# Optimization experiments

Measured on AMD Instinct MI355X. Metric: run time of the kernel, lower is better.

Reference implementation:

```python
import jax, jax.numpy as jnp
import numpy as np

E_DIM = 640   # RNA-FM embedding dim
H = 256       # hidden_dim
L = 3         # num_gcn_layers
LN_EPS = 1e-5


def _layer_norm(x, g, b):
    mu = jnp.mean(x, axis=-1, keepdims=True)
    var = jnp.mean((x - mu) ** 2, axis=-1, keepdims=True)
    return (x - mu) * jax.lax.rsqrt(var + LN_EPS) * g + b


def setup_inputs() -> dict:
    key = jax.random.key(0)
    ks = jax.random.split(key, 20)
    B, S = 4, 256

    def w(k, shape):
        fan_in = shape[-2] if len(shape) >= 2 else shape[-1]
        return jax.random.normal(k, shape, dtype=jnp.float32) / np.sqrt(fan_in)

    inp = {
        "embeddings": jax.random.normal(ks[0], (B, S, E_DIM), dtype=jnp.float32),
        "bp_priors": jax.random.uniform(ks[1], (B, S, S), dtype=jnp.float32),
        "sequence_lengths": jnp.full((B,), S, dtype=jnp.int32),
        # FeatureEncoder: Linear(640, 512) -> ReLU -> Linear(512, 256)
        "enc_w1": w(ks[2], (E_DIM, 2 * H)), "enc_b1": jnp.zeros((2 * H,), jnp.float32),
        "enc_w2": w(ks[3], (2 * H, H)),     "enc_b2": jnp.zeros((H,), jnp.float32),
        # GCN layers (stacked over L)
        "gcn_wself": w(ks[4], (L, H, H)), "gcn_bself": jnp.zeros((L, H), jnp.float32),
        "gcn_wedge": w(ks[5], (L, H, H)), "gcn_bedge": jnp.zeros((L, H), jnp.float32),
        "gcn_ln_g": jnp.ones((L, H), jnp.float32), "gcn_ln_b": jnp.zeros((L, H), jnp.float32),
        # PairwiseScorer MLP: Linear(2H+1, H) -> ReLU -> Linear(H, H//2) -> ReLU -> Linear(H//2, 1)
        "mlp_w1": w(ks[6], (2 * H + 1, H)), "mlp_b1": jnp.zeros((H,), jnp.float32),
        "mlp_w2": w(ks[7], (H, H // 2)),    "mlp_b2": jnp.zeros((H // 2,), jnp.float32),
        "mlp_w3": w(ks[8], (H // 2, 1)),    "mlp_b3": jnp.zeros((1,), jnp.float32),
    }
    return inp


def reference(embeddings, bp_priors, sequence_lengths,
              enc_w1, enc_b1, enc_w2, enc_b2,
              gcn_wself, gcn_bself, gcn_wedge, gcn_bedge, gcn_ln_g, gcn_ln_b,
              mlp_w1, mlp_b1, mlp_w2, mlp_b2, mlp_w3, mlp_b3):
    # FeatureEncoder
    h = jax.nn.relu(embeddings @ enc_w1 + enc_b1) @ enc_w2 + enc_b2  # [B,S,H]

    # GCN layers: self GEMM + adjacency (bp_priors) aggregated neighbor GEMM
    for l in range(L):
        self_f = h @ gcn_wself[l] + gcn_bself[l]
        neigh_f = jnp.einsum('bij,bjh->bih', bp_priors, h @ gcn_wedge[l] + gcn_bedge[l])
        h = _layer_norm(jax.nn.relu(self_f + neigh_f), gcn_ln_g[l], gcn_ln_b[l])

    # PairwiseScorer: concat([node_i, node_j, prior]) @ W1 split into three partial products
    # (mathematically identical to the expand-concat-MLP in the torch module).
    hi = h @ mlp_w1[:H]           # [B,S,H] contribution of node_i
    hj = h @ mlp_w1[H:2 * H]      # [B,S,H] contribution of node_j
    p = jax.nn.relu(hi[:, :, None, :] + hj[:, None, :, :]
                    + bp_priors[..., None] * mlp_w1[2 * H] + mlp_b1)  # [B,S,S,H]
    p = jax.nn.relu(p @ mlp_w2 + mlp_b2)                              # [B,S,S,H//2]
    bp_scores = (p @ mlp_w3 + mlp_b3)[..., 0]                         # [B,S,S]
    return bp_scores
```

## Files before the change

### kernel.cpp

```cpp
#include <hip/hip_runtime.h>

typedef __attribute__((ext_vector_type(8))) short short8;
typedef __attribute__((ext_vector_type(4))) float f32x4;

__device__ __forceinline__ unsigned short f2bf(float x) {
    union { float f; unsigned u; } v; v.f = x;
    unsigned r = v.u + 0x7FFF + ((v.u >> 16) & 1);
    return (unsigned short)(r >> 16);
}
__device__ __forceinline__ float bf2f(unsigned short h) {
    union { unsigned u; float f; } v; v.u = ((unsigned)h) << 16;
    return v.f;
}

template<bool RELU>
__global__ __launch_bounds__(256)
void gemm32(const float* __restrict__ A, const float* __restrict__ B0,
            const float* __restrict__ bias0, float* __restrict__ C0,
            const float* __restrict__ B1, const float* __restrict__ bias1,
            float* __restrict__ C1,
            int M, int N, int K, int aB, int bB, int cB, int nxHalf)
{
    int bx = blockIdx.x;
    const float* B = B0; const float* bias = bias0; float* C = C0;
    if (nxHalf && bx >= nxHalf) { bx -= nxHalf; B = B1; bias = bias1; C = C1; }
    A += (long)blockIdx.z * aB;
    B += (long)blockIdx.z * bB;
    C += (long)blockIdx.z * cB;
    const int m0 = blockIdx.y * 32, n0 = bx * 64;

    __shared__ __align__(16) float As[32][36];
    __shared__ __align__(16) float Bs[32][68];
    const int tid = threadIdx.x;
    const int tx = tid & 15, ty = tid >> 4;
    float acc[2][4] = {};

    for (int k0 = 0; k0 < K; k0 += 32) {
        {
            int row = tid >> 3, kq = (tid & 7) << 2;
            float4 v = *(const float4*)&A[(long)(m0 + row) * K + k0 + kq];
            As[kq + 0][row] = v.x; As[kq + 1][row] = v.y;
            As[kq + 2][row] = v.z; As[kq + 3][row] = v.w;
        }
#pragma unroll
        for (int q = 0; q < 2; ++q) {
            int f = tid * 2 + q;
            int kk = f >> 4, nn = (f & 15) << 2;
            *(float4*)&Bs[kk][nn] = *(const float4*)&B[(long)(k0 + kk) * N + n0 + nn];
        }
        __syncthreads();
#pragma unroll
        for (int k = 0; k < 32; ++k) {
            float2 a2 = *(const float2*)&As[k][ty * 2];
            float4 b4 = *(const float4*)&Bs[k][tx * 4];
            acc[0][0] += a2.x * b4.x; acc[0][1] += a2.x * b4.y;
            acc[0][2] += a2.x * b4.z; acc[0][3] += a2.x * b4.w;
            acc[1][0] += a2.y * b4.x; acc[1][1] += a2.y * b4.y;
            acc[1][2] += a2.y * b4.z; acc[1][3] += a2.y * b4.w;
        }
        __syncthreads();
    }

#pragma unroll
    for (int i = 0; i < 2; ++i) {
        int m = m0 + ty * 2 + i;
#pragma unroll
        for (int j = 0; j < 4; ++j) {
            int n = n0 + tx * 4 + j;
            float v = acc[i][j];
            if (bias) v += bias[n];
            if (RELU) v = fmaxf(v, 0.f);
            C[(long)m * N + n] = v;
        }
    }
}

__global__ __launch_bounds__(256)
void add_relu_ln(const float* __restrict__ a, const float* __restrict__ b,
                 const float* __restrict__ g, const float* __restrict__ bb,
                 float* __restrict__ o)
{
    const int row = blockIdx.x, t = threadIdx.x;
    const long idx = (long)row * 256 + t;
    float x = fmaxf(a[idx] + b[idx], 0.f);
    float s = x, s2 = x * x;
#pragma unroll
    for (int off = 1; off < 64; off <<= 1) {
        s  += __shfl_xor(s,  off, 64);
        s2 += __shfl_xor(s2, off, 64);
    }
    __shared__ float ws1[4], ws2[4];
    const int wid = t >> 6, lane = t & 63;
    if (lane == 0) { ws1[wid] = s; ws2[wid] = s2; }
    __syncthreads();
    s  = ws1[0] + ws1[1] + ws1[2] + ws1[3];
    s2 = ws2[0] + ws2[1] + ws2[2] + ws2[3];
    const float mu  = s * (1.f / 256.f);
    const float var = s2 * (1.f / 256.f) - mu * mu;
    o[idx] = (x - mu) * rsqrtf(var + 1e-5f) * g[t] + bb[t];
}

__global__ __launch_bounds__(256)
void split_w2t(const float* __restrict__ w2, short* __restrict__ w2th,
               short* __restrict__ w2tl)
{
    int e = blockIdx.x * 256 + threadIdx.x;
    int k = e >> 7, n = e & 127;
    float x = w2[k * 128 + n];
    unsigned short h = f2bf(x);
    unsigned short lo = f2bf(x - bf2f(h));
    w2th[n * 256 + k] = (short)h;
    w2tl[n * 256 + k] = (short)lo;
}

__global__ __launch_bounds__(256)
void pairwise_mfma(const float* __restrict__ hia, const float* __restrict__ hja,
                   const float* __restrict__ bp,
                   const float* __restrict__ c,
                   const float* __restrict__ b1,
                   const short* __restrict__ w2th, const short* __restrict__ w2tl,
                   const float* __restrict__ b2,
                   const float* __restrict__ w3,
                   const float* __restrict__ b3,
                   float* __restrict__ out)
{
    const int b = blockIdx.z, ib0 = blockIdx.y * 2, jb = blockIdx.x;
    const int tid = threadIdx.x;
    const int l = tid & 63, wid = tid >> 6;
    const int wm0 = (wid & 1) * 64, wn0 = (wid >> 1) * 64;

    __shared__ __align__(16) short Ph[128 * 32];
    __shared__ __align__(16) short Pl[128 * 32];
    __shared__ __align__(16) float hjs[64][36];
    __shared__ __align__(16) float his[2][36];
    __shared__ __align__(16) float cs[32];
    __shared__ __align__(16) float b1s[32];
    __shared__ float bpv[128];
    __shared__ float red[128][2];

    if (tid < 128) {
        int i = ib0 + (tid >> 6), j = jb * 64 + (tid & 63);
        bpv[tid] = bp[((long)(b * 256 + i)) * 256 + j];
    }

    f32x4 acc[4][4] = {};

    for (int kt = 0; kt < 8; ++kt) {
        const int k0 = kt * 32;
#pragma unroll
        for (int q = 0; q < 2; ++q) {
            int f = tid * 2 + q;
            int row = f >> 3, kq = (f & 7) << 2;
            *(float4*)&hjs[row][kq] =
                *(const float4*)&hja[((long)(b * 256 + jb * 64 + row)) * 256 + k0 + kq];
        }
        if (tid < 16) {
            int row = tid >> 3, kq = (tid & 7) << 2;
            *(float4*)&his[row][kq] =
                *(const float4*)&hia[((long)(b * 256 + ib0 + row)) * 256 + k0 + kq];
        } else if (tid < 24) {
            int f = tid - 16;
            *(float4*)&cs[f * 4] = *(const float4*)&c[k0 + f * 4];
        } else if (tid < 32) {
            int f = tid - 24;
            *(float4*)&b1s[f * 4] = *(const float4*)&b1[k0 + f * 4];
        }
        __syncthreads();

        {
            const int p = tid >> 1, kb = (tid & 1) << 4;
            const int ii = p >> 6, jj = p & 63;
            const float bw = bpv[p];
            const int swz = (p & 7) << 4;
            char* phc = (char*)Ph;
            char* plc = (char*)Pl;
#pragma unroll
            for (int q = 0; q < 4; ++q) {
                float4 hv = *(const float4*)&hjs[jj][kb + q * 4];
                float4 iv = *(const float4*)&his[ii][kb + q * 4];
                float4 cv = *(const float4*)&cs[kb + q * 4];
                float4 bv = *(const float4*)&b1s[kb + q * 4];
                float xs[4];
                xs[0] = fmaxf(iv.x + hv.x + bw * cv.x + bv.x, 0.f);
                xs[1] = fmaxf(iv.y + hv.y + bw * cv.y + bv.y, 0.f);
                xs[2] = fmaxf(iv.z + hv.z + bw * cv.z + bv.z, 0.f);
                xs[3] = fmaxf(iv.w + hv.w + bw * cv.w + bv.w, 0.f);
                unsigned hw[4], lw[4];
#pragma unroll
                for (int e = 0; e < 4; ++e) {
                    unsigned short hh = f2bf(xs[e]);
                    unsigned short ll = f2bf(xs[e] - bf2f(hh));
                    hw[e] = hh; lw[e] = ll;
                }
                int base = p * 64 + (kb + q * 4) * 2;
                *(unsigned*)(phc + ((base    ) ^ swz)) = hw[0] | (hw[1] << 16);
                *(unsigned*)(phc + ((base + 4) ^ swz)) = hw[2] | (hw[3] << 16);
                *(unsigned*)(plc + ((base    ) ^ swz)) = lw[0] | (lw[1] << 16);
                *(unsigned*)(plc + ((base + 4) ^ swz)) = lw[2] | (lw[3] << 16);
            }
        }
        __syncthreads();

        short8 ah[4], al[4], bh[4], bl[4];
        const int g = l >> 4, ln = l & 15;
#pragma unroll
        for (int mf = 0; mf < 4; ++mf) {
            int row = wm0 + mf * 16 + ln;
            int off = (row * 64 + g * 16) ^ ((row & 7) << 4);
            ah[mf] = *(const short8*)((const char*)Ph + off);
            al[mf] = *(const short8*)((const char*)Pl + off);
        }
#pragma unroll
        for (int nf = 0; nf < 4; ++nf) {
            int col = wn0 + nf * 16 + ln;
            long boff = (long)col * 256 + k0 + g * 8;
            bh[nf] = *(const short8*)(w2th + boff);
            bl[nf] = *(const short8*)(w2tl + boff);
        }
#pragma unroll
        for (int mf = 0; mf < 4; ++mf)
#pragma unroll
            for (int nf = 0; nf < 4; ++nf) {
                acc[mf][nf] = __builtin_amdgcn_mfma_f32_16x16x32_bf16(
                    ah[mf], bh[nf], acc[mf][nf], 0, 0, 0);
                acc[mf][nf] = __builtin_amdgcn_mfma_f32_16x16x32_bf16(
                    ah[mf], bl[nf], acc[mf][nf], 0, 0, 0);
                acc[mf][nf] = __builtin_amdgcn_mfma_f32_16x16x32_bf16(
                    al[mf], bh[nf], acc[mf][nf], 0, 0, 0);
            }
        __syncthreads();
    }

    const int g = l >> 4, ln = l & 15;
    float b2v[4], w3v[4];
#pragma unroll
    for (int nf = 0; nf < 4; ++nf) {
        int col = wn0 + nf * 16 + ln;
        b2v[nf] = b2[col];
        w3v[nf] = w3[col];
    }
#pragma unroll
    for (int mf = 0; mf < 4; ++mf) {
#pragma unroll
        for (int r = 0; r < 4; ++r) {
            float s = 0.f;
#pragma unroll
            for (int nf = 0; nf < 4; ++nf)
                s += fmaxf(acc[mf][nf][r] + b2v[nf], 0.f) * w3v[nf];
            s += __shfl_xor(s, 1, 64);
            s += __shfl_xor(s, 2, 64);
            s += __shfl_xor(s, 4, 64);
            s += __shfl_xor(s, 8, 64);
            if (ln == 0)
                red[wm0 + mf * 16 + g * 4 + r][wid >> 1] = s;
        }
    }
    __syncthreads();
    if (tid < 128) {
        int i = ib0 + (tid >> 6), j = jb * 64 + (tid & 63);
        out[((long)(b * 256 + i)) * 256 + j] = red[tid][0] + red[tid][1] + b3[0];
    }
}

extern "C" void kernel_launch(void* const* d_in, const int* in_sizes, int n_in,
                              void* d_out, int out_size, void* d_ws, size_t ws_size,
                              hipStream_t stream)
{
    const float* emb   = (const float*)d_in[0];
    const float* bp    = (const float*)d_in[1];
    const float* ew1   = (const float*)d_in[3];
    const float* eb1   = (const float*)d_in[4];
    const float* ew2   = (const float*)d_in[5];
    const float* eb2   = (const float*)d_in[6];
    const float* wself = (const float*)d_in[7];
    const float* bself = (const float*)d_in[8];
    const float* wedge = (const float*)d_in[9];
    const float* bedge = (const float*)d_in[10];
    const float* lng   = (const float*)d_in[11];
    const float* lnb   = (const float*)d_in[12];
    const float* mw1   = (const float*)d_in[13];
    const float* mb1   = (const float*)d_in[14];
    const float* mw2   = (const float*)d_in[15];
    const float* mb2   = (const float*)d_in[16];
    const float* mw3   = (const float*)d_in[17];
    const float* mb3   = (const float*)d_in[18];
    float* out = (float*)d_out;

    float* ws = (float*)d_ws;
    float* h1 = ws;
    float* h  = h1 + 524288;
    float* sf = h  + 262144;
    float* eg = sf + 262144;
    float* ng = eg + 262144;
    float* hi = ng + 262144;
    float* hj = hi + 262144;
    short* w2th = (short*)h1;
    short* w2tl = w2th + 32768;

    dim3 blk(256);

    gemm32<true ><<<dim3(8, 32, 1), blk, 0, stream>>>(emb, ew1, eb1, h1,
        nullptr, nullptr, nullptr, 1024, 512, 640, 0, 0, 0, 0);
    gemm32<false><<<dim3(4, 32, 1), blk, 0, stream>>>(h1, ew2, eb2, h,
        nullptr, nullptr, nullptr, 1024, 256, 512, 0, 0, 0, 0);

    split_w2t<<<dim3(128), blk, 0, stream>>>(mw2, w2th, w2tl);

    for (int lyr = 0; lyr < 3; ++lyr) {
        gemm32<false><<<dim3(8, 32, 1), blk, 0, stream>>>(h,
            wself + lyr * 65536, bself + lyr * 256, sf,
            wedge + lyr * 65536, bedge + lyr * 256, eg,
            1024, 256, 256, 0, 0, 0, 4);
        gemm32<false><<<dim3(4, 8, 4), blk, 0, stream>>>(bp, eg, nullptr, ng,
            nullptr, nullptr, nullptr, 256, 256, 256, 65536, 65536, 65536, 0);
        add_relu_ln<<<dim3(1024), blk, 0, stream>>>(sf, ng,
            lng + lyr * 256, lnb + lyr * 256, h);
    }

    gemm32<false><<<dim3(8, 32, 1), blk, 0, stream>>>(h,
        mw1, nullptr, hi, mw1 + 65536, nullptr, hj,
        1024, 256, 256, 0, 0, 0, 4);

    pairwise_mfma<<<dim3(4, 128, 4), blk, 0, stream>>>(hi, hj, bp,
        mw1 + 131072, mb1, w2th, w2tl, mb2, mw3, mb3, out);
}
```

Measured before the change: 353.7 us.

## Fuse encoder and GCN stages into persistent megakernel; restructure pairwise MFMA kernel

All encoder, GCN and projection GEMMs plus layer norms now run in one persistent kernel of 512 blocks, separated by hand-written grid barriers built on atomics. This replaces about a dozen separate kernel launches. The pairwise kernel is also rebuilt: the first-layer activations are computed directly in registers in MFMA fragment layout instead of being staged through LDS, hj tiles are double-buffered with global_load_lds and an XOR swizzle, and the bf16 hi/lo split uses truncation instead of rounding. The grid barrier assumes all 512 blocks are resident at the same time, so it can deadlock if occupancy is lower. Truncating the split also changes numerics slightly.

```diff
diff --git a/kernel.cpp b/kernel.cpp
--- a/kernel.cpp
+++ b/kernel.cpp
@@ -3,56 +3,55 @@
 typedef __attribute__((ext_vector_type(8))) short short8;
 typedef __attribute__((ext_vector_type(4))) float f32x4;
 
-__device__ __forceinline__ unsigned short f2bf(float x) {
-    union { float f; unsigned u; } v; v.f = x;
-    unsigned r = v.u + 0x7FFF + ((v.u >> 16) & 1);
-    return (unsigned short)(r >> 16);
-}
-__device__ __forceinline__ float bf2f(unsigned short h) {
-    union { unsigned u; float f; } v; v.u = ((unsigned)h) << 16;
-    return v.f;
-}
-
-template<bool RELU>
-__global__ __launch_bounds__(256)
-void gemm32(const float* __restrict__ A, const float* __restrict__ B0,
-            const float* __restrict__ bias0, float* __restrict__ C0,
-            const float* __restrict__ B1, const float* __restrict__ bias1,
-            float* __restrict__ C1,
-            int M, int N, int K, int aB, int bB, int cB, int nxHalf)
-{
-    int bx = blockIdx.x;
-    const float* B = B0; const float* bias = bias0; float* C = C0;
-    if (nxHalf && bx >= nxHalf) { bx -= nxHalf; B = B1; bias = bias1; C = C1; }
-    A += (long)blockIdx.z * aB;
-    B += (long)blockIdx.z * bB;
-    C += (long)blockIdx.z * cB;
-    const int m0 = blockIdx.y * 32, n0 = bx * 64;
-
-    __shared__ __align__(16) float As[32][36];
-    __shared__ __align__(16) float Bs[32][68];
+__device__ __forceinline__ void gload_lds16(const void* g, void* l) {
+    __builtin_amdgcn_global_load_lds(
+        (const __attribute__((address_space(1))) unsigned*)g,
+        (__attribute__((address_space(3))) unsigned*)l, 16, 0, 0);
+}
+#define MFMA16(a, b, c) __builtin_amdgcn_mfma_f32_16x16x32_bf16((a), (b), (c), 0, 0, 0)
+
+#define BAR_STRIDE 144
+__device__ __forceinline__ void gridbar(unsigned* base) {
+    __threadfence();
+    __syncthreads();
+    if (threadIdx.x == 0) {
+        unsigned* sub = base + 16 + (blockIdx.x & 7) * 16;
+        unsigned prev = atomicAdd(sub, 1u);
+        if (prev == 63u) atomicAdd(base, 1u);
+        while (__hip_atomic_load(base, __ATOMIC_RELAXED, __HIP_MEMORY_SCOPE_AGENT) < 8u)
+            __builtin_amdgcn_s_sleep(2);
+    }
+    __syncthreads();
+    __threadfence();
+}
+
+__device__ __forceinline__
+void gemm_dev(const float* __restrict__ A, const float* __restrict__ B,
+              const float* __restrict__ bias, float* __restrict__ C,
+              int N, int K, int m0, int n0, bool relu,
+              float* As, float* Bs)
+{
     const int tid = threadIdx.x;
     const int tx = tid & 15, ty = tid >> 4;
     float acc[2][4] = {};
-
     for (int k0 = 0; k0 < K; k0 += 32) {
         {
             int row = tid >> 3, kq = (tid & 7) << 2;
             float4 v = *(const float4*)&A[(long)(m0 + row) * K + k0 + kq];
-            As[kq + 0][row] = v.x; As[kq + 1][row] = v.y;
-            As[kq + 2][row] = v.z; As[kq + 3][row] = v.w;
+            As[(kq + 0) * 36 + row] = v.x; As[(kq + 1) * 36 + row] = v.y;
+            As[(kq + 2) * 36 + row] = v.z; As[(kq + 3) * 36 + row] = v.w;
         }
 #pragma unroll
         for (int q = 0; q < 2; ++q) {
             int f = tid * 2 + q;
             int kk = f >> 4, nn = (f & 15) << 2;
-            *(float4*)&Bs[kk][nn] = *(const float4*)&B[(long)(k0 + kk) * N + n0 + nn];
+            *(float4*)&Bs[kk * 68 + nn] = *(const float4*)&B[(long)(k0 + kk) * N + n0 + nn];
         }
         __syncthreads();
 #pragma unroll
         for (int k = 0; k < 32; ++k) {
-            float2 a2 = *(const float2*)&As[k][ty * 2];
-            float4 b4 = *(const float4*)&Bs[k][tx * 4];
+            float2 a2 = *(const float2*)&As[k * 36 + ty * 2];
+            float4 b4 = *(const float4*)&Bs[k * 68 + tx * 4];
             acc[0][0] += a2.x * b4.x; acc[0][1] += a2.x * b4.y;
             acc[0][2] += a2.x * b4.z; acc[0][3] += a2.x * b4.w;
             acc[1][0] += a2.y * b4.x; acc[1][1] += a2.y * b4.y;
@@ -60,7 +59,6 @@
         }
         __syncthreads();
     }
-
 #pragma unroll
     for (int i = 0; i < 2; ++i) {
         int m = m0 + ty * 2 + i;
@@ -69,169 +67,209 @@
             int n = n0 + tx * 4 + j;
             float v = acc[i][j];
             if (bias) v += bias[n];
-            if (RELU) v = fmaxf(v, 0.f);
+            if (relu) v = fmaxf(v, 0.f);
             C[(long)m * N + n] = v;
         }
     }
 }
 
-__global__ __launch_bounds__(256)
-void add_relu_ln(const float* __restrict__ a, const float* __restrict__ b,
-                 const float* __restrict__ g, const float* __restrict__ bb,
-                 float* __restrict__ o)
-{
-    const int row = blockIdx.x, t = threadIdx.x;
+__device__ __forceinline__
+void ln_dev(const float* __restrict__ a, const float* __restrict__ bsrc,
+            const float* __restrict__ g, const float* __restrict__ bb,
+            float* __restrict__ o, int row, float* scratch)
+{
+    const int t = threadIdx.x;
     const long idx = (long)row * 256 + t;
-    float x = fmaxf(a[idx] + b[idx], 0.f);
+    float x = fmaxf(a[idx] + bsrc[idx], 0.f);
     float s = x, s2 = x * x;
 #pragma unroll
     for (int off = 1; off < 64; off <<= 1) {
         s  += __shfl_xor(s,  off, 64);
         s2 += __shfl_xor(s2, off, 64);
     }
-    __shared__ float ws1[4], ws2[4];
-    const int wid = t >> 6, lane = t & 63;
-    if (lane == 0) { ws1[wid] = s; ws2[wid] = s2; }
-    __syncthreads();
-    s  = ws1[0] + ws1[1] + ws1[2] + ws1[3];
-    s2 = ws2[0] + ws2[1] + ws2[2] + ws2[3];
+    const int wd = t >> 6, lane = t & 63;
+    __syncthreads();
+    if (lane == 0) { scratch[wd] = s; scratch[4 + wd] = s2; }
+    __syncthreads();
+    s  = scratch[0] + scratch[1] + scratch[2] + scratch[3];
+    s2 = scratch[4] + scratch[5] + scratch[6] + scratch[7];
     const float mu  = s * (1.f / 256.f);
     const float var = s2 * (1.f / 256.f) - mu * mu;
     o[idx] = (x - mu) * rsqrtf(var + 1e-5f) * g[t] + bb[t];
 }
 
-__global__ __launch_bounds__(256)
-void split_w2t(const float* __restrict__ w2, short* __restrict__ w2th,
-               short* __restrict__ w2tl)
-{
-    int e = blockIdx.x * 256 + threadIdx.x;
-    int k = e >> 7, n = e & 127;
-    float x = w2[k * 128 + n];
-    unsigned short h = f2bf(x);
-    unsigned short lo = f2bf(x - bf2f(h));
-    w2th[n * 256 + k] = (short)h;
-    w2tl[n * 256 + k] = (short)lo;
-}
-
-__global__ __launch_bounds__(256)
-void pairwise_mfma(const float* __restrict__ hia, const float* __restrict__ hja,
-                   const float* __restrict__ bp,
-                   const float* __restrict__ c,
-                   const float* __restrict__ b1,
-                   const short* __restrict__ w2th, const short* __restrict__ w2tl,
-                   const float* __restrict__ b2,
-                   const float* __restrict__ w3,
-                   const float* __restrict__ b3,
-                   float* __restrict__ out)
-{
-    const int b = blockIdx.z, ib0 = blockIdx.y * 2, jb = blockIdx.x;
-    const int tid = threadIdx.x;
-    const int l = tid & 63, wid = tid >> 6;
+__global__ __launch_bounds__(256, 2)
+void mega(const float* __restrict__ emb, const float* __restrict__ bpm,
+          const float* __restrict__ ew1, const float* __restrict__ eb1,
+          const float* __restrict__ ew2, const float* __restrict__ eb2,
+          const float* __restrict__ wself, const float* __restrict__ bself,
+          const float* __restrict__ wedge, const float* __restrict__ bedge,
+          const float* __restrict__ lng, const float* __restrict__ lnb,
+          const float* __restrict__ mw1, const float* __restrict__ mw2,
+          float* __restrict__ h1, float* __restrict__ h,
+          float* __restrict__ sf, float* __restrict__ eg, float* __restrict__ ng,
+          float* __restrict__ hi, float* __restrict__ hj,
+          short* __restrict__ w2th, short* __restrict__ w2tl,
+          unsigned* __restrict__ bars)
+{
+    __shared__ __align__(16) float As[32 * 36];
+    __shared__ __align__(16) float Bs[32 * 68];
+    const int blk = blockIdx.x;
+    int ib = 0;
+
+    if (blk < 256) {
+        gemm_dev(emb, ew1, eb1, h1, 512, 640, (blk >> 3) * 32, (blk & 7) * 64, true, As, Bs);
+    } else {
+        int e = (blk - 256) * 256 + threadIdx.x;
+        if (e < 32768) {
+            int k = e >> 7, n = e & 127;
+            float x = mw2[e];
+            unsigned hu = __float_as_uint(x) & 0xFFFF0000u;
+            w2th[n * 256 + k] = (short)(hu >> 16);
+            w2tl[n * 256 + k] = (short)(__float_as_uint(x - __uint_as_float(hu)) >> 16);
+        }
+    }
+    gridbar(bars + (ib++) * BAR_STRIDE);
+
+    if (blk < 128)
+        gemm_dev(h1, ew2, eb2, h, 256, 512, (blk >> 2) * 32, (blk & 3) * 64, false, As, Bs);
+    gridbar(bars + (ib++) * BAR_STRIDE);
+
+    for (int l = 0; l < 3; ++l) {
+        if (blk < 128)
+            gemm_dev(h, wself + l * 65536, bself + l * 256, sf, 256, 256,
+                     (blk >> 2) * 32, (blk & 3) * 64, false, As, Bs);
+        else if (blk < 256) {
+            int t = blk - 128;
+            gemm_dev(h, wedge + l * 65536, bedge + l * 256, eg, 256, 256,
+                     (t >> 2) * 32, (t & 3) * 64, false, As, Bs);
+        }
+        gridbar(bars + (ib++) * BAR_STRIDE);
+
+        if (blk < 128) {
+            int bb = blk >> 5, r = blk & 31;
+            gemm_dev(bpm + bb * 65536, eg + bb * 65536, nullptr, ng + bb * 65536,
+                     256, 256, (r >> 2) * 32, (r & 3) * 64, false, As, Bs);
+        }
+        gridbar(bars + (ib++) * BAR_STRIDE);
+
+        ln_dev(sf, ng, lng + l * 256, lnb + l * 256, h, blk * 2, As);
+        ln_dev(sf, ng, lng + l * 256, lnb + l * 256, h, blk * 2 + 1, As);
+        gridbar(bars + (ib++) * BAR_STRIDE);
+    }
+
+    if (blk < 128)
+        gemm_dev(h, mw1, nullptr, hi, 256, 256, (blk >> 2) * 32, (blk & 3) * 64, false, As, Bs);
+    else if (blk < 256) {
+        int t = blk - 128;
+        gemm_dev(h, mw1 + 65536, nullptr, hj, 256, 256, (t >> 2) * 32, (t & 3) * 64, false, As, Bs);
+    }
+}
+
+__global__ __launch_bounds__(256, 3)
+void pairwise2(const float* __restrict__ hia, const float* __restrict__ hja,
+               const float* __restrict__ bpm,
+               const float* __restrict__ c, const float* __restrict__ b1,
+               const short* __restrict__ w2th, const short* __restrict__ w2tl,
+               const float* __restrict__ b2, const float* __restrict__ w3,
+               const float* __restrict__ b3, float* __restrict__ out)
+{
+    const int b = blockIdx.z, ib0 = blockIdx.y * 2, j0 = blockIdx.x * 64;
+    const int tid = threadIdx.x, l = tid & 63, wid = tid >> 6;
     const int wm0 = (wid & 1) * 64, wn0 = (wid >> 1) * 64;
-
-    __shared__ __align__(16) short Ph[128 * 32];
-    __shared__ __align__(16) short Pl[128 * 32];
-    __shared__ __align__(16) float hjs[64][36];
-    __shared__ __align__(16) float his[2][36];
-    __shared__ __align__(16) float cs[32];
-    __shared__ __align__(16) float b1s[32];
-    __shared__ float bpv[128];
+    const int g = l >> 4, ln = l & 15;
+    const int ii = wid & 1;
+
+    __shared__ __align__(16) float hjs[2][64 * 32];
+    __shared__ __align__(16) float hib[2][256];
+    __shared__ __align__(16) float csv[256];
     __shared__ float red[128][2];
 
-    if (tid < 128) {
-        int i = ib0 + (tid >> 6), j = jb * 64 + (tid & 63);
-        bpv[tid] = bp[((long)(b * 256 + i)) * 256 + j];
-    }
+    {
+        int i2 = tid >> 7, kk = (tid & 127) * 2;
+        float2 hv = *(const float2*)&hia[((long)(b * 256 + ib0 + i2)) * 256 + kk];
+        float2 bv = *(const float2*)&b1[kk];
+        hib[i2][kk] = hv.x + bv.x; hib[i2][kk + 1] = hv.y + bv.y;
+        if (tid < 64) *(float4*)&csv[tid * 4] = *(const float4*)&c[tid * 4];
+    }
+    float bw[4];
+#pragma unroll
+    for (int mf = 0; mf < 4; ++mf)
+        bw[mf] = bpm[((long)(b * 256 + ib0 + ii)) * 256 + j0 + mf * 16 + ln];
+
+    {
+        int row = tid >> 3, q = tid & 7;
+        gload_lds16(&hja[((long)(b * 256 + j0 + row)) * 256 + (q ^ (row & 7)) * 4],
+                    (char*)&hjs[0][0] + tid * 16);
+        int row2 = 32 + row;
+        gload_lds16(&hja[((long)(b * 256 + j0 + row2)) * 256 + (q ^ (row2 & 7)) * 4],
+                    (char*)&hjs[0][0] + 4096 + tid * 16);
+    }
+    __syncthreads();
 
     f32x4 acc[4][4] = {};
 
     for (int kt = 0; kt < 8; ++kt) {
-        const int k0 = kt * 32;
-#pragma unroll
-        for (int q = 0; q < 2; ++q) {
-            int f = tid * 2 + q;
-            int row = f >> 3, kq = (f & 7) << 2;
-            *(float4*)&hjs[row][kq] =
-                *(const float4*)&hja[((long)(b * 256 + jb * 64 + row)) * 256 + k0 + kq];
-        }
-        if (tid < 16) {
-            int row = tid >> 3, kq = (tid & 7) << 2;
-            *(float4*)&his[row][kq] =
-                *(const float4*)&hia[((long)(b * 256 + ib0 + row)) * 256 + k0 + kq];
-        } else if (tid < 24) {
-            int f = tid - 16;
-            *(float4*)&cs[f * 4] = *(const float4*)&c[k0 + f * 4];
-        } else if (tid < 32) {
-            int f = tid - 24;
-            *(float4*)&b1s[f * 4] = *(const float4*)&b1[k0 + f * 4];
-        }
-        __syncthreads();
-
-        {
-            const int p = tid >> 1, kb = (tid & 1) << 4;
-            const int ii = p >> 6, jj = p & 63;
-            const float bw = bpv[p];
-            const int swz = (p & 7) << 4;
-            char* phc = (char*)Ph;
-            char* plc = (char*)Pl;
-#pragma unroll
-            for (int q = 0; q < 4; ++q) {
-                float4 hv = *(const float4*)&hjs[jj][kb + q * 4];
-                float4 iv = *(const float4*)&his[ii][kb + q * 4];
-                float4 cv = *(const float4*)&cs[kb + q * 4];
-                float4 bv = *(const float4*)&b1s[kb + q * 4];
-                float xs[4];
-                xs[0] = fmaxf(iv.x + hv.x + bw * cv.x + bv.x, 0.f);
-                xs[1] = fmaxf(iv.y + hv.y + bw * cv.y + bv.y, 0.f);
-                xs[2] = fmaxf(iv.z + hv.z + bw * cv.z + bv.z, 0.f);
-                xs[3] = fmaxf(iv.w + hv.w + bw * cv.w + bv.w, 0.f);
-                unsigned hw[4], lw[4];
-#pragma unroll
-                for (int e = 0; e < 4; ++e) {
-                    unsigned short hh = f2bf(xs[e]);
-                    unsigned short ll = f2bf(xs[e] - bf2f(hh));
-                    hw[e] = hh; lw[e] = ll;
-                }
-                int base = p * 64 + (kb + q * 4) * 2;
-                *(unsigned*)(phc + ((base    ) ^ swz)) = hw[0] | (hw[1] << 16);
-                *(unsigned*)(phc + ((base + 4) ^ swz)) = hw[2] | (hw[3] << 16);
-                *(unsigned*)(plc + ((base    ) ^ swz)) = lw[0] | (lw[1] << 16);
-                *(unsigned*)(plc + ((base + 4) ^ swz)) = lw[2] | (lw[3] << 16);
-            }
-        }
-        __syncthreads();
-
-        short8 ah[4], al[4], bh[4], bl[4];
-        const int g = l >> 4, ln = l & 15;
-#pragma unroll
-        for (int mf = 0; mf < 4; ++mf) {
-            int row = wm0 + mf * 16 + ln;
-            int off = (row * 64 + g * 16) ^ ((row & 7) << 4);
-            ah[mf] = *(const short8*)((const char*)Ph + off);
-            al[mf] = *(const short8*)((const char*)Pl + off);
-        }
+        const int cur = kt & 1;
+        if (kt < 7) {
+            int row = tid >> 3, q = tid & 7;
+            gload_lds16(&hja[((long)(b * 256 + j0 + row)) * 256 + (kt + 1) * 32
+                             + (q ^ (row & 7)) * 4],
+                        (char*)&hjs[cur ^ 1][0] + tid * 16);
+            int row2 = 32 + row;
+            gload_lds16(&hja[((long)(b * 256 + j0 + row2)) * 256 + (kt + 1) * 32
+                             + (q ^ (row2 & 7)) * 4],
+                        (char*)&hjs[cur ^ 1][0] + 4096 + tid * 16);
+        }
+        short8 bh[4], bl[4];
 #pragma unroll
         for (int nf = 0; nf < 4; ++nf) {
             int col = wn0 + nf * 16 + ln;
-            long boff = (long)col * 256 + k0 + g * 8;
-            bh[nf] = *(const short8*)(w2th + boff);
-            bl[nf] = *(const short8*)(w2tl + boff);
-        }
-#pragma unroll
-        for (int mf = 0; mf < 4; ++mf)
+            long bo = (long)col * 256 + kt * 32 + g * 8;
+            bh[nf] = *(const short8*)(w2th + bo);
+            bl[nf] = *(const short8*)(w2tl + bo);
+        }
+        float hv8[8], cv8[8];
+        *(float4*)&hv8[0] = *(const float4*)&hib[ii][kt * 32 + g * 8];
+        *(float4*)&hv8[4] = *(const float4*)&hib[ii][kt * 32 + g * 8 + 4];
+        *(float4*)&cv8[0] = *(const float4*)&csv[kt * 32 + g * 8];
+        *(float4*)&cv8[4] = *(const float4*)&csv[kt * 32 + g * 8 + 4];
+
+#pragma unroll
+        for (int mf = 0; mf < 4; ++mf) {
+            const int jj = mf * 16 + ln;
+            const int rowbase = jj * 128;
+            const int sw = (jj & 7) << 4;
+            float hjv[8];
+            *(float4*)&hjv[0] = *(const float4*)((const char*)&hjs[cur][0]
+                                                 + rowbase + ((g * 32) ^ sw));
+            *(float4*)&hjv[4] = *(const float4*)((const char*)&hjs[cur][0]
+                                                 + rowbase + ((g * 32 + 16) ^ sw));
+            unsigned ph[4], pl[4];
+#pragma unroll
+            for (int e = 0; e < 4; ++e) {
+                float x0 = fmaxf(fmaf(bw[mf], cv8[2 * e],     hv8[2 * e])     + hjv[2 * e],     0.f);
+                float x1 = fmaxf(fmaf(bw[mf], cv8[2 * e + 1], hv8[2 * e + 1]) + hjv[2 * e + 1], 0.f);
+                unsigned u0 = __float_as_uint(x0), u1 = __float_as_uint(x1);
+                unsigned h0 = u0 & 0xFFFF0000u, h1 = u1 & 0xFFFF0000u;
+                ph[e] = (h0 >> 16) | h1;
+                unsigned l0 = __float_as_uint(x0 - __uint_as_float(h0));
+                unsigned l1 = __float_as_uint(x1 - __uint_as_float(h1));
+                pl[e] = (l0 >> 16) | (l1 & 0xFFFF0000u);
+            }
+            union { unsigned u[4]; short8 s; } ua, ul;
+            ua.u[0] = ph[0]; ua.u[1] = ph[1]; ua.u[2] = ph[2]; ua.u[3] = ph[3];
+            ul.u[0] = pl[0]; ul.u[1] = pl[1]; ul.u[2] = pl[2]; ul.u[3] = pl[3];
 #pragma unroll
             for (int nf = 0; nf < 4; ++nf) {
-                acc[mf][nf] = __builtin_amdgcn_mfma_f32_16x16x32_bf16(
-                    ah[mf], bh[nf], acc[mf][nf], 0, 0, 0);
-                acc[mf][nf] = __builtin_amdgcn_mfma_f32_16x16x32_bf16(
-                    ah[mf], bl[nf], acc[mf][nf], 0, 0, 0);
-                acc[mf][nf] = __builtin_amdgcn_mfma_f32_16x16x32_bf16(
-                    al[mf], bh[nf], acc[mf][nf], 0, 0, 0);
+                acc[mf][nf] = MFMA16(ua.s, bh[nf], acc[mf][nf]);
+                acc[mf][nf] = MFMA16(ua.s, bl[nf], acc[mf][nf]);
+                acc[mf][nf] = MFMA16(ul.s, bh[nf], acc[mf][nf]);
             }
+        }
         __syncthreads();
     }
 
-    const int g = l >> 4, ln = l & 15;
     float b2v[4], w3v[4];
 #pragma unroll
     for (int nf = 0; nf < 4; ++nf) {
@@ -257,7 +295,7 @@
     }
     __syncthreads();
     if (tid < 128) {
-        int i = ib0 + (tid >> 6), j = jb * 64 + (tid & 63);
+        int i = ib0 + (tid >> 6), j = j0 + (tid & 63);
         out[((long)(b * 256 + i)) * 256 + j] = red[tid][0] + red[tid][1] + b3[0];
     }
 }
@@ -267,7 +305,7 @@
                               hipStream_t stream)
 {
     const float* emb   = (const float*)d_in[0];
-    const float* bp    = (const float*)d_in[1];
+    const float* bpm   = (const float*)d_in[1];
     const float* ew1   = (const float*)d_in[3];
     const float* eb1   = (const float*)d_in[4];
     const float* ew2   = (const float*)d_in[5];
@@ -294,33 +332,16 @@
     float* ng = eg + 262144;
     float* hi = ng + 262144;
     float* hj = hi + 262144;
-    short* w2th = (short*)h1;
+    short* w2th = (short*)(hj + 262144);
     short* w2tl = w2th + 32768;
-
-    dim3 blk(256);
-
-    gemm32<true ><<<dim3(8, 32, 1), blk, 0, stream>>>(emb, ew1, eb1, h1,
-        nullptr, nullptr, nullptr, 1024, 512, 640, 0, 0, 0, 0);
-    gemm32<false><<<dim3(4, 32, 1), blk, 0, stream>>>(h1, ew2, eb2, h,
-        nullptr, nullptr, nullptr, 1024, 256, 512, 0, 0, 0, 0);
-
-    split_w2t<<<dim3(128), blk, 0, stream>>>(mw2, w2th, w2tl);
-
-    for (int lyr = 0; lyr < 3; ++lyr) {
-        gemm32<false><<<dim3(8, 32, 1), blk, 0, stream>>>(h,
-            wself + lyr * 65536, bself + lyr * 256, sf,
-            wedge + lyr * 65536, bedge + lyr * 256, eg,
-            1024, 256, 256, 0, 0, 0, 4);
-        gemm32<false><<<dim3(4, 8, 4), blk, 0, stream>>>(bp, eg, nullptr, ng,
-            nullptr, nullptr, nullptr, 256, 256, 256, 65536, 65536, 65536, 0);
-        add_relu_ln<<<dim3(1024), blk, 0, stream>>>(sf, ng,
-            lng + lyr * 256, lnb + lyr * 256, h);
-    }
-
-    gemm32<false><<<dim3(8, 32, 1), blk, 0, stream>>>(h,
-        mw1, nullptr, hi, mw1 + 65536, nullptr, hj,
-        1024, 256, 256, 0, 0, 0, 4);
-
-    pairwise_mfma<<<dim3(4, 128, 4), blk, 0, stream>>>(hi, hj, bp,
-        mw1 + 131072, mb1, w2th, w2tl, mb2, mw3, mb3, out);
-}
+    unsigned* bars = (unsigned*)(w2tl + 32768);
+
+    hipMemsetAsync(bars, 0, 11 * BAR_STRIDE * sizeof(unsigned), stream);
+
+    mega<<<dim3(512), dim3(256), 0, stream>>>(
+        emb, bpm, ew1, eb1, ew2, eb2, wself, bself, wedge, bedge,
+        lng, lnb, mw1, mw2, h1, h, sf, eg, ng, hi, hj, w2th, w2tl, bars);
+
+    pairwise2<<<dim3(4, 128, 4), dim3(256), 0, stream>>>(
+        hi, hj, bpm, mw1 + 131072, mb1, w2th, w2tl, mb2, mw3, mb3, out);
+}
```

After: 1.096 ms. 3.1x slower.
